# Kernel tuning notes

Measured on AMD Instinct MI355X. Metric: run time of the kernel, lower is better.

## Reference

```python
import jax, jax.numpy as jnp
import numpy as np

B, T, C = 2, 2048, 1024
H, DH = 16, 64            # n_head, head_size; H*DH == C
HID = 4096                # FFN hidden
EPS = 1e-5


def setup_inputs() -> dict:
    key = jax.random.key(0)
    ks = jax.random.split(key, 16)
    s_c = 1.0 / np.sqrt(C)
    s_h = 1.0 / np.sqrt(HID)
    return {
        "x": jax.random.normal(ks[0], (B, T, C), jnp.float32),
        "ln1_g": jnp.ones((C,), jnp.float32),
        "ln1_b": jnp.zeros((C,), jnp.float32),
        "Wq": jax.random.normal(ks[1], (H, C, DH), jnp.float32) * s_c,
        "Wk": jax.random.normal(ks[2], (H, C, DH), jnp.float32) * s_c,
        "Wv": jax.random.normal(ks[3], (H, C, DH), jnp.float32) * s_c,
        "Wo": jax.random.normal(ks[4], (C, C), jnp.float32) * s_c,
        "bo": jnp.zeros((C,), jnp.float32),
        "ln2_g": jnp.ones((C,), jnp.float32),
        "ln2_b": jnp.zeros((C,), jnp.float32),
        "W1": jax.random.normal(ks[5], (C, HID), jnp.float32) * s_c,
        "b1": jnp.zeros((HID,), jnp.float32),
        "W2": jax.random.normal(ks[6], (HID, C), jnp.float32) * s_h,
        "b2": jnp.zeros((C,), jnp.float32),
    }


def _layernorm(x, g, b):
    mu = jnp.mean(x, axis=-1, keepdims=True)
    var = jnp.mean(jnp.square(x - mu), axis=-1, keepdims=True)
    return (x - mu) * jax.lax.rsqrt(var + EPS) * g + b


def _block(x, ln1_g, ln1_b, Wq, Wk, Wv, Wo, bo, ln2_g, ln2_b, W1, b1, W2, b2):
    # --- self-attention (note: scale by C**-0.5, as in original code) ---
    h = _layernorm(x, ln1_g, ln1_b)                      # [B,T,C]
    q = jnp.einsum("btc,hcd->bhtd", h, Wq)
    k = jnp.einsum("btc,hcd->bhtd", h, Wk)
    v = jnp.einsum("btc,hcd->bhtd", h, Wv)
    wei = jnp.einsum("bhtd,bhsd->bhts", q, k) * (C ** -0.5)
    causal = jnp.tril(jnp.ones((T, T), bool))            # [T,T]
    wei = jnp.where(causal, wei, -jnp.inf)
    wei = jax.nn.softmax(wei, axis=-1)
    att = jnp.einsum("bhts,bhsd->bhtd", wei, v)          # [B,H,T,DH]
    att = att.transpose(0, 2, 1, 3).reshape(x.shape[0], x.shape[1], C)  # concat heads
    x = x + att @ Wo + bo
    # --- feed-forward ---
    h2 = _layernorm(x, ln2_g, ln2_b)
    x = x + jax.nn.relu(h2 @ W1 + b1) @ W2 + b2
    return x


def reference(x, ln1_g, ln1_b, Wq, Wk, Wv, Wo, bo, ln2_g, ln2_b, W1, b1, W2, b2):
    return _block(x, ln1_g, ln1_b, Wq, Wk, Wv, Wo, bo, ln2_g, ln2_b, W1, b1, W2, b2)
```

## Files before the change

kernel.cpp:

```cpp
#include <hip/hip_runtime.h>

typedef unsigned short ushort_t;
typedef __attribute__((ext_vector_type(8))) short short8;
typedef __attribute__((ext_vector_type(4))) float f32x4;

#define BT 4096
#define TSEQ 2048
#define CC 1024
#define NH 16
#define DH 64
#define HID 4096
#define ATT_SCALE 0.03125f

__device__ __forceinline__ ushort_t f2bf(float f) {
    unsigned u = __float_as_uint(f);
    u = u + 0x7fffu + ((u >> 16) & 1u);
    return (ushort_t)(u >> 16);
}
__device__ __forceinline__ float bf2f(ushort_t u) {
    return __uint_as_float(((unsigned)u) << 16);
}

typedef const __attribute__((address_space(1))) unsigned int* gptr_t;
typedef __attribute__((address_space(3))) unsigned int* lptr_t;
__device__ __forceinline__ void gload_lds16(const void* g, void* l) {
    __builtin_amdgcn_global_load_lds((gptr_t)g, (lptr_t)l, 16, 0, 0);
}

template <int N> __device__ __forceinline__ void vmcnt_wait() {
    if constexpr (N == 0)      asm volatile("s_waitcnt vmcnt(0)" ::: "memory");
    else if constexpr (N == 3) asm volatile("s_waitcnt vmcnt(3)" ::: "memory");
    else if constexpr (N == 4) asm volatile("s_waitcnt vmcnt(4)" ::: "memory");
    else if constexpr (N == 6) asm volatile("s_waitcnt vmcnt(6)" ::: "memory");
    else if constexpr (N == 8) asm volatile("s_waitcnt vmcnt(8)" ::: "memory");
    else static_assert(N == 0, "unsupported vmcnt");
}

__global__ __launch_bounds__(256) void transpose_cvt(
    const float* __restrict__ in, ushort_t* __restrict__ out, int R, int Cn)
{
    __shared__ float tile[32][33];
    size_t off = (size_t)blockIdx.z * R * Cn;
    int c0 = blockIdx.x * 32, r0 = blockIdx.y * 32;
    int tx = threadIdx.x & 31, ty = threadIdx.x >> 5;
#pragma unroll
    for (int q = 0; q < 4; ++q)
        tile[ty + 8 * q][tx] = in[off + (size_t)(r0 + ty + 8 * q) * Cn + c0 + tx];
    __syncthreads();
#pragma unroll
    for (int q = 0; q < 4; ++q)
        out[off + (size_t)(c0 + ty + 8 * q) * R + r0 + tx] = f2bf(tile[tx][ty + 8 * q]);
}

__global__ __launch_bounds__(256) void transpose_qkv(
    const float* __restrict__ Wq, const float* __restrict__ Wk,
    const float* __restrict__ Wv, ushort_t* __restrict__ WqkvT)
{
    __shared__ float tile[32][33];
    int z = blockIdx.z, mat = z >> 4, head = z & 15;
    const float* in = (mat == 0 ? Wq : (mat == 1 ? Wk : Wv)) + (size_t)head * CC * DH;
    ushort_t* out = WqkvT + (size_t)z * DH * CC;
    int c0 = blockIdx.x * 32, r0 = blockIdx.y * 32;
    int tx = threadIdx.x & 31, ty = threadIdx.x >> 5;
#pragma unroll
    for (int q = 0; q < 4; ++q)
        tile[ty + 8 * q][tx] = in[(size_t)(r0 + ty + 8 * q) * DH + c0 + tx];
    __syncthreads();
#pragma unroll
    for (int q = 0; q < 4; ++q)
        out[(size_t)(c0 + ty + 8 * q) * CC + r0 + tx] = f2bf(tile[tx][ty + 8 * q]);
}

__global__ __launch_bounds__(256) void ln_kernel(
    const float* __restrict__ x, const float* __restrict__ g,
    const float* __restrict__ b, ushort_t* __restrict__ out)
{
    int row = blockIdx.x;
    const float4 xv = ((const float4*)(x + (size_t)row * CC))[threadIdx.x];
    float s = xv.x + xv.y + xv.z + xv.w;
    float s2 = xv.x * xv.x + xv.y * xv.y + xv.z * xv.z + xv.w * xv.w;
#pragma unroll
    for (int d = 1; d < 64; d <<= 1) {
        s += __shfl_xor(s, d);
        s2 += __shfl_xor(s2, d);
    }
    __shared__ float ps[4], ps2[4];
    int w = threadIdx.x >> 6, lane = threadIdx.x & 63;
    if (lane == 0) { ps[w] = s; ps2[w] = s2; }
    __syncthreads();
    s = ps[0] + ps[1] + ps[2] + ps[3];
    s2 = ps2[0] + ps2[1] + ps2[2] + ps2[3];
    float mu = s * (1.0f / CC);
    float var = s2 * (1.0f / CC) - mu * mu;
    float rs = rsqrtf(var + 1e-5f);
    int c = threadIdx.x * 4;
    const float4 gv = ((const float4*)g)[threadIdx.x];
    const float4 bv = ((const float4*)b)[threadIdx.x];
    ushort_t u0 = f2bf((xv.x - mu) * rs * gv.x + bv.x);
    ushort_t u1 = f2bf((xv.y - mu) * rs * gv.y + bv.y);
    ushort_t u2 = f2bf((xv.z - mu) * rs * gv.z + bv.z);
    ushort_t u3 = f2bf((xv.w - mu) * rs * gv.w + bv.w);
    unsigned lo = (unsigned)u0 | ((unsigned)u1 << 16);
    unsigned hi = (unsigned)u2 | ((unsigned)u3 << 16);
    ((uint2*)(out + (size_t)row * CC + c))[0] = make_uint2(lo, hi);
}

template <int BM, int BN, int WM, int WN, int MR, int NR, int MODE, int D>
__global__ __launch_bounds__(256) void gemm_tile(
    const ushort_t* __restrict__ A, const ushort_t* __restrict__ Bt,
    int N, int K, int lda, int ldb,
    const float* __restrict__ bias, const float* __restrict__ resid,
    void* __restrict__ out0, void* __restrict__ out1, void* __restrict__ out2)
{
    static_assert(WM * WN == 4 && WM * MR * 16 == BM && WN * NR * 16 == BN, "geom");
    constexpr int L = BM / 64 + BN / 64;
    __shared__ ushort_t As[D][BM * 32];
    __shared__ ushort_t Bs[D][BN * 32];

    const int t = threadIdx.x;
    const int w = t >> 6, lane = t & 63, g = lane >> 4, c = lane & 15;
    const int wr = w / WN, wc = w % WN;
    const int m0 = blockIdx.x * BM;
    const int n0 = blockIdx.y * BN;
    if (MODE == 3) {
        A += (size_t)blockIdx.z * K;
        Bt += (size_t)blockIdx.z * K;
    }

    f32x4 acc[MR][NR];
#pragma unroll
    for (int mi = 0; mi < MR; ++mi)
#pragma unroll
        for (int ni = 0; ni < NR; ++ni) acc[mi][ni] = f32x4{0.f, 0.f, 0.f, 0.f};

    const int arow = t >> 2, acol = (t & 3) * 8;
    const int aoff = (wr * MR * 16 + c) * 32 + g * 8;
    const int boff = (wc * NR * 16 + c) * 32 + g * 8;

#define STAGE(BUF, K0)                                                          \
    {                                                                           \
        _Pragma("unroll") for (int j = 0; j < BM / 64; ++j)                     \
            gload_lds16(A + (size_t)(m0 + j * 64 + arow) * lda + (K0) + acol,   \
                        As[BUF] + (size_t)j * 2048 + t * 8);                    \
        _Pragma("unroll") for (int j = 0; j < BN / 64; ++j)                     \
            gload_lds16(Bt + (size_t)(n0 + j * 64 + arow) * ldb + (K0) + acol,  \
                        Bs[BUF] + (size_t)j * 2048 + t * 8);                    \
    }

    const int nt = K >> 5;
#pragma unroll
    for (int d = 0; d < D - 1; ++d) STAGE(d, d * 32);

    int cur = 0;
    for (int ti = 0; ti < nt; ++ti) {
        const int ahead = nt - 1 - ti;
        if (ahead >= D - 1) {
            const int stg = (cur == 0) ? D - 1 : cur - 1;
            STAGE(stg, (ti + D - 1) * 32);
            vmcnt_wait<(D - 1) * L>();
        } else if (D == 3 && ahead == 1) {
            vmcnt_wait<L>();
        } else {
            vmcnt_wait<0>();
        }
        __builtin_amdgcn_sched_barrier(0);
        __builtin_amdgcn_s_barrier();

        const ushort_t* Ard = As[cur] + aoff;
        const ushort_t* Brd = Bs[cur] + boff;
        short8 af[MR], bf[NR];
#pragma unroll
        for (int mi = 0; mi < MR; ++mi) af[mi] = *(const short8*)(Ard + mi * 512);
#pragma unroll
        for (int ni = 0; ni < NR; ++ni) bf[ni] = *(const short8*)(Brd + ni * 512);
        __builtin_amdgcn_s_setprio(1);
#pragma unroll
        for (int mi = 0; mi < MR; ++mi)
#pragma unroll
            for (int ni = 0; ni < NR; ++ni)
                acc[mi][ni] = __builtin_amdgcn_mfma_f32_16x16x32_bf16(
                    af[mi], bf[ni], acc[mi][ni], 0, 0, 0);
        __builtin_amdgcn_s_setprio(0);

        __builtin_amdgcn_sched_barrier(0);
        __builtin_amdgcn_s_barrier();
        cur = (cur + 1 == D) ? 0 : cur + 1;
    }
#undef STAGE

#pragma unroll
    for (int mi = 0; mi < MR; ++mi)
#pragma unroll
        for (int ni = 0; ni < NR; ++ni)
#pragma unroll
            for (int i = 0; i < 4; ++i) {
                int row = m0 + wr * MR * 16 + mi * 16 + g * 4 + i;
                int col = n0 + wc * NR * 16 + ni * 16 + c;
                float v = acc[mi][ni][i];
                if (MODE == 0) {
                    v += bias[col] + resid[(size_t)row * N + col];
                    ((float*)out0)[(size_t)row * N + col] = v;
                } else if (MODE == 1) {
                    v += bias[col];
                    v = v > 0.f ? v : 0.f;
                    ((ushort_t*)out0)[(size_t)row * N + col] = f2bf(v);
                } else if (MODE == 3) {
                    ((ushort_t*)out0)[(size_t)blockIdx.z * BT * N + (size_t)row * N + col] =
                        f2bf(v);
                } else {
                    int bb = row >> 11, tt = row & (TSEQ - 1);
                    if (col < 1024) {
                        int head = col >> 6, d = col & 63;
                        ((ushort_t*)out0)[((size_t)(bb * NH + head) * TSEQ + tt) * DH + d] =
                            f2bf(v * ATT_SCALE);
                    } else if (col < 2048) {
                        int head = (col - 1024) >> 6, d = col & 63;
                        ((ushort_t*)out1)[((size_t)(bb * NH + head) * TSEQ + tt) * DH + d] = f2bf(v);
                    } else {
                        int head = (col - 2048) >> 6, d = col & 63;
                        ((ushort_t*)out2)[((size_t)(bb * NH + head) * DH + d) * TSEQ + tt] = f2bf(v);
                    }
                }
            }
}

__global__ __launch_bounds__(256) void ffn2_combine(
    const ushort_t* __restrict__ parts, const float* __restrict__ bias,
    const float* __restrict__ resid, float* __restrict__ out)
{
    const size_t off = ((size_t)blockIdx.x * 256 + threadIdx.x) * 8;
    const int col = (int)(off & 1023);
    short8 p0 = *(const short8*)(parts + off);
    short8 p1 = *(const short8*)(parts + (size_t)BT * CC + off);
    float4 r0 = ((const float4*)(resid + off))[0];
    float4 r1 = ((const float4*)(resid + off + 4))[0];
    float4 b0 = ((const float4*)(bias + col))[0];
    float4 b1 = ((const float4*)(bias + col + 4))[0];
    float o[8];
#pragma unroll
    for (int j = 0; j < 8; ++j)
        o[j] = bf2f((ushort_t)p0[j]) + bf2f((ushort_t)p1[j]);
    float4 w0 = make_float4(o[0] + b0.x + r0.x, o[1] + b0.y + r0.y,
                            o[2] + b0.z + r0.z, o[3] + b0.w + r0.w);
    float4 w1 = make_float4(o[4] + b1.x + r1.x, o[5] + b1.y + r1.y,
                            o[6] + b1.z + r1.z, o[7] + b1.w + r1.w);
    ((float4*)(out + off))[0] = w0;
    ((float4*)(out + off + 4))[0] = w1;
}

__global__ __launch_bounds__(256) void flash_split(
    const ushort_t* __restrict__ Q, const ushort_t* __restrict__ Kb,
    const ushort_t* __restrict__ Vt, float* __restrict__ opart,
    float* __restrict__ mlpart, ushort_t* __restrict__ attout)
{
    __shared__ ushort_t Ks[64 * 64];
    __shared__ ushort_t Vs[64 * 64];
    __shared__ ushort_t Plds[4][16 * 72];
    const int t = threadIdx.x;
    const int w = t >> 6, lane = t & 63;
    const int g = lane >> 4, c = lane & 15;
    const int bh = blockIdx.x, qb = blockIdx.y, sc = blockIdx.z;
    if (sc * 8 > qb) return;
    const int bb = bh >> 4, hh = bh & 15;
    const int q0 = qb * 64 + w * 16;
    const ushort_t* qp = Q + (size_t)bh * TSEQ * DH;
    const char* kpB = (const char*)(Kb + (size_t)bh * TSEQ * DH);
    const char* vpB = (const char*)(Vt + (size_t)bh * DH * TSEQ);

    const short8 bq0 = *(const short8*)(qp + (size_t)(q0 + c) * DH + g * 8);
    const short8 bq1 = *(const short8*)(qp + (size_t)(q0 + c) * DH + 32 + g * 8);

    float m_ = -INFINITY, l_ = 0.f;
    f32x4 o[4];
#pragma unroll
    for (int nf = 0; nf < 4; ++nf) o[nf] = f32x4{0.f, 0.f, 0.f, 0.f};

    const int st0 = sc * 8;
    const int send = (st0 + 7 < qb) ? st0 + 7 : qb;
    ushort_t* pw = &Plds[w][c * 72];
    const unsigned bxor = (unsigned)((c & 7) << 4);

    const int srow = t >> 3, sb = (t & 7) * 16;
#define STAGE_KV(ST)                                                                \
    {                                                                               \
        const int S0_ = (ST) * 64;                                                  \
        _Pragma("unroll") for (int j = 0; j < 2; ++j) {                             \
            int r = j * 32 + srow;                                                  \
            int bs = sb ^ ((r & 7) << 4);                                           \
            gload_lds16(kpB + (size_t)(S0_ + r) * 128 + bs,                         \
                        (char*)Ks + r * 128 + sb);                                  \
            gload_lds16(vpB + (size_t)r * (TSEQ * 2) + S0_ * 2 + bs,                \
                        (char*)Vs + r * 128 + sb);                                  \
        }                                                                           \
    }

    STAGE_KV(st0);
    for (int st = st0; st <= send; ++st) {
        const int S0 = st * 64;
        __syncthreads();

        __builtin_amdgcn_s_setprio(1);
        f32x4 sa[4];
#pragma unroll
        for (int sub = 0; sub < 4; ++sub) {
            const char* kr = (const char*)Ks + (16 * sub + c) * 128;
            short8 k0 = *(const short8*)(kr + ((g * 16) ^ bxor));
            short8 k1 = *(const short8*)(kr + ((64 + g * 16) ^ bxor));
            f32x4 t0 = f32x4{0.f, 0.f, 0.f, 0.f};
            t0 = __builtin_amdgcn_mfma_f32_16x16x32_bf16(k0, bq0, t0, 0, 0, 0);
            t0 = __builtin_amdgcn_mfma_f32_16x16x32_bf16(k1, bq1, t0, 0, 0, 0);
            sa[sub] = t0;
        }
        __builtin_amdgcn_s_setprio(0);

        float pvv[16];
#pragma unroll
        for (int sub = 0; sub < 4; ++sub)
#pragma unroll
            for (int i = 0; i < 4; ++i) pvv[4 * sub + i] = sa[sub][i];
        if (st == qb) {
#pragma unroll
            for (int sub = 0; sub < 4; ++sub)
#pragma unroll
                for (int i = 0; i < 4; ++i)
                    if (S0 + 16 * sub + 4 * g + i > q0 + c) pvv[4 * sub + i] = -INFINITY;
        }
        float tmax = pvv[0];
#pragma unroll
        for (int j = 1; j < 16; ++j) tmax = fmaxf(tmax, pvv[j]);
        tmax = fmaxf(tmax, __shfl_xor(tmax, 16));
        tmax = fmaxf(tmax, __shfl_xor(tmax, 32));
        if (!__all(tmax - m_ <= 8.0f)) {
            float mn = fmaxf(m_, tmax);
            float fac = __expf(m_ - mn);
            m_ = mn;
            l_ *= fac;
#pragma unroll
            for (int i = 0; i < 4; ++i) {
                float fr = __shfl(fac, 4 * g + i);
#pragma unroll
                for (int nf = 0; nf < 4; ++nf) o[nf][i] *= fr;
            }
        }
        float pp[16], rs = 0.f;
#pragma unroll
        for (int j = 0; j < 16; ++j) { pp[j] = __expf(pvv[j] - m_); rs += pp[j]; }
        rs += __shfl_xor(rs, 16);
        rs += __shfl_xor(rs, 32);
        l_ += rs;

#pragma unroll
        for (int sub = 0; sub < 4; ++sub) {
            unsigned lo = (__float_as_uint(pp[4 * sub + 0]) >> 16) |
                          (__float_as_uint(pp[4 * sub + 1]) & 0xffff0000u);
            unsigned hi = (__float_as_uint(pp[4 * sub + 2]) >> 16) |
                          (__float_as_uint(pp[4 * sub + 3]) & 0xffff0000u);
            *(uint2*)(pw + 16 * sub + 4 * g) = make_uint2(lo, hi);
        }
        asm volatile("s_waitcnt lgkmcnt(0)" ::: "memory");
        short8 pa0 = *(const short8*)(&Plds[w][c * 72 + g * 8]);
        short8 pa1 = *(const short8*)(&Plds[w][c * 72 + 32 + g * 8]);

        __builtin_amdgcn_s_setprio(1);
#pragma unroll
        for (int nf = 0; nf < 4; ++nf) {
            const char* vr = (const char*)Vs + (nf * 16 + c) * 128;
            short8 v0 = *(const short8*)(vr + ((g * 16) ^ bxor));
            short8 v1 = *(const short8*)(vr + ((64 + g * 16) ^ bxor));
            o[nf] = __builtin_amdgcn_mfma_f32_16x16x32_bf16(pa0, v0, o[nf], 0, 0, 0);
            o[nf] = __builtin_amdgcn_mfma_f32_16x16x32_bf16(pa1, v1, o[nf], 0, 0, 0);
        }
        __builtin_amdgcn_s_setprio(0);

        __syncthreads();
        if (st < send) STAGE_KV(st + 1);
    }
#undef STAGE_KV

    if (qb < 8) {
#pragma unroll
        for (int i = 0; i < 4; ++i) {
            float rl = 1.0f / __shfl(l_, 4 * g + i);
            int tt = q0 + 4 * g + i;
#pragma unroll
            for (int nf = 0; nf < 4; ++nf)
                attout[((size_t)(bb * TSEQ + tt)) * CC + hh * DH + nf * 16 + c] =
                    f2bf(o[nf][i] * rl);
        }
    } else {
        const size_t slot = (size_t)(bh * 32 + qb) * 4 + sc;
        float* op = opart + slot * 4096;
#pragma unroll
        for (int nf = 0; nf < 4; ++nf)
#pragma unroll
            for (int i = 0; i < 4; ++i)
                op[(size_t)(w * 16 + 4 * g + i) * 64 + nf * 16 + c] = o[nf][i];
        if (g == 0) {
            mlpart[slot * 128 + w * 16 + c] = m_;
            mlpart[slot * 128 + 64 + w * 16 + c] = l_;
        }
    }
}

__global__ __launch_bounds__(256) void flash_combine(
    const float* __restrict__ opart, const float* __restrict__ mlpart,
    ushort_t* __restrict__ attout)
{
    const int bh = blockIdx.x, qb = blockIdx.y + 8;
    const int bb = bh >> 4, hh = bh & 15;
    const int nsc = (qb >> 3) + 1;
    const int t = threadIdx.x, r = t >> 2, qc = t & 3;
    const size_t slot0 = (size_t)(bh * 32 + qb) * 4;

    float mi[4], li[4];
    float M = -INFINITY;
#pragma unroll
    for (int i = 0; i < 4; ++i) {
        if (i < nsc) {
            mi[i] = mlpart[(slot0 + i) * 128 + r];
            li[i] = mlpart[(slot0 + i) * 128 + 64 + r];
            M = fmaxf(M, mi[i]);
        }
    }
    float L = 0.f;
    f32x4 acc[4];
#pragma unroll
    for (int j = 0; j < 4; ++j) acc[j] = f32x4{0.f, 0.f, 0.f, 0.f};
#pragma unroll
    for (int i = 0; i < 4; ++i) {
        if (i < nsc) {
            float F = __expf(mi[i] - M);
            L += li[i] * F;
            const f32x4* orow = (const f32x4*)(opart + (slot0 + i) * 4096 +
                                               (size_t)r * 64 + qc * 16);
#pragma unroll
            for (int j = 0; j < 4; ++j) acc[j] += orow[j] * F;
        }
    }
    float rl = 1.0f / L;
    unsigned wb[8];
#pragma unroll
    for (int j = 0; j < 4; ++j) {
        wb[2 * j] = (unsigned)f2bf(acc[j][0] * rl) | ((unsigned)f2bf(acc[j][1] * rl) << 16);
        wb[2 * j + 1] = (unsigned)f2bf(acc[j][2] * rl) | ((unsigned)f2bf(acc[j][3] * rl) << 16);
    }
    ushort_t* dst = attout + ((size_t)(bb * TSEQ + qb * 64 + r)) * CC + hh * DH + qc * 16;
    ((uint4*)dst)[0] = make_uint4(wb[0], wb[1], wb[2], wb[3]);
    ((uint4*)dst)[1] = make_uint4(wb[4], wb[5], wb[6], wb[7]);
}

extern "C" void kernel_launch(void* const* d_in, const int* in_sizes, int n_in,
                              void* d_out, int out_size, void* d_ws, size_t ws_size,
                              hipStream_t stream)
{
    (void)in_sizes; (void)n_in; (void)out_size; (void)ws_size;
    const float* x     = (const float*)d_in[0];
    const float* ln1_g = (const float*)d_in[1];
    const float* ln1_b = (const float*)d_in[2];
    const float* Wq    = (const float*)d_in[3];
    const float* Wk    = (const float*)d_in[4];
    const float* Wv    = (const float*)d_in[5];
    const float* Wo    = (const float*)d_in[6];
    const float* bo    = (const float*)d_in[7];
    const float* ln2_g = (const float*)d_in[8];
    const float* ln2_b = (const float*)d_in[9];
    const float* W1    = (const float*)d_in[10];
    const float* b1    = (const float*)d_in[11];
    const float* W2    = (const float*)d_in[12];
    const float* b2    = (const float*)d_in[13];

    char* p = (char*)d_ws;
    ushort_t* hbuf  = (ushort_t*)p;  p += (size_t)BT * CC * 2;
    ushort_t* WqkvT = (ushort_t*)p;  p += (size_t)3 * CC * CC * 2;
    ushort_t* WoT   = (ushort_t*)p;  p += (size_t)CC * CC * 2;
    ushort_t* W1T   = (ushort_t*)p;  p += (size_t)CC * HID * 2;
    ushort_t* W2T   = (ushort_t*)p;  p += (size_t)HID * CC * 2;
    ushort_t* Qb    = (ushort_t*)p;  p += (size_t)BT * CC * 2;
    ushort_t* Kbuf  = (ushort_t*)p;  p += (size_t)BT * CC * 2;
    ushort_t* Vt    = (ushort_t*)p;  p += (size_t)BT * CC * 2;
    ushort_t* atto  = (ushort_t*)p;  p += (size_t)BT * CC * 2;
    float*    x1    = (float*)p;     p += (size_t)BT * CC * 4;
    ushort_t* h2    = (ushort_t*)p;  p += (size_t)BT * CC * 2;
    ushort_t* mid   = (ushort_t*)p;  p += (size_t)BT * HID * 2;
    float*    opart = (float*)p;     p += (size_t)4096 * 4096 * 4;
    float*    mlprt = (float*)p;     p += (size_t)4096 * 128 * 4;

    dim3 blk(256);
    transpose_qkv<<<dim3(DH / 32, CC / 32, 3 * NH), blk, 0, stream>>>(Wq, Wk, Wv, WqkvT);
    transpose_cvt<<<dim3(CC / 32, CC / 32, 1), blk, 0, stream>>>(Wo, WoT, CC, CC);
    transpose_cvt<<<dim3(HID / 32, CC / 32, 1), blk, 0, stream>>>(W1, W1T, CC, HID);
    transpose_cvt<<<dim3(CC / 32, HID / 32, 1), blk, 0, stream>>>(W2, W2T, HID, CC);

    ln_kernel<<<dim3(BT), blk, 0, stream>>>(x, ln1_g, ln1_b, hbuf);
    gemm_tile<128, 128, 2, 2, 4, 4, 2, 2><<<dim3(BT / 128, 3072 / 128), blk, 0, stream>>>(
        hbuf, WqkvT, 3072, CC, CC, CC, nullptr, nullptr, Qb, Kbuf, Vt);
    flash_split<<<dim3(2 * NH, TSEQ / 64, 4), blk, 0, stream>>>(
        Qb, Kbuf, Vt, opart, mlprt, atto);
    flash_combine<<<dim3(2 * NH, TSEQ / 64 - 8), blk, 0, stream>>>(opart, mlprt, atto);
    gemm_tile<128, 64, 4, 1, 2, 4, 0, 3><<<dim3(BT / 128, CC / 64), blk, 0, stream>>>(
        atto, WoT, CC, CC, CC, CC, bo, x, (void*)x1, nullptr, nullptr);
    ln_kernel<<<dim3(BT), blk, 0, stream>>>(x1, ln2_g, ln2_b, h2);
    gemm_tile<128, 128, 2, 2, 4, 4, 1, 2><<<dim3(BT / 128, HID / 128), blk, 0, stream>>>(
        h2, W1T, HID, CC, CC, CC, b1, nullptr, (void*)mid, nullptr, nullptr);
    gemm_tile<128, 64, 4, 1, 2, 4, 3, 3><<<dim3(BT / 128, CC / 64, 2), blk, 0, stream>>>(
        mid, W2T, CC, HID / 2, HID, HID, nullptr, nullptr, (void*)opart, nullptr, nullptr);
    ffn2_combine<<<dim3(BT * CC / 8 / 256), blk, 0, stream>>>(
        (const ushort_t*)opart, b2, x1, (float*)d_out);
}
```

Measured before the change: 253.5 us.

## Add 256x256 XOR-swizzled 512-thread GEMM for QKV, FFN1 and split-K FFN2

Adds a new GEMM kernel with 256x256 output tiles, 512 threads (8 waves), BK=64 double buffering, and an XOR-swizzled LDS layout that avoids bank conflicts. It is used for the QKV projection, FFN up-projection and FFN down-projection. The down-projection split-K goes from 2 to 4 splits so the grid stays large enough, and the combine kernel now sums four bf16 partials. The bigger tiles raise data reuse per block, at the cost of more registers and LDS per block, fewer blocks for the smaller GEMMs, and an extra partial-sum read and bf16 rounding in the combine step.

```diff
diff --git a/kernel.cpp b/kernel.cpp
--- a/kernel.cpp
+++ b/kernel.cpp
@@ -105,102 +105,114 @@
     ((uint2*)(out + (size_t)row * CC + c))[0] = make_uint2(lo, hi);
 }
 
-template <int BM, int BN, int WM, int WN, int MR, int NR, int MODE, int D>
-__global__ __launch_bounds__(256) void gemm_tile(
+template <int MODE>
+__global__ __launch_bounds__(512) void gemm256(
     const ushort_t* __restrict__ A, const ushort_t* __restrict__ Bt,
-    int N, int K, int lda, int ldb,
-    const float* __restrict__ bias, const float* __restrict__ resid,
+    int N, int K, int lda, int ldb, const float* __restrict__ bias,
     void* __restrict__ out0, void* __restrict__ out1, void* __restrict__ out2)
 {
-    static_assert(WM * WN == 4 && WM * MR * 16 == BM && WN * NR * 16 == BN, "geom");
-    constexpr int L = BM / 64 + BN / 64;
-    __shared__ ushort_t As[D][BM * 32];
-    __shared__ ushort_t Bs[D][BN * 32];
+    __shared__ ushort_t As[2][256 * 64];
+    __shared__ ushort_t Bs[2][256 * 64];
 
     const int t = threadIdx.x;
-    const int w = t >> 6, lane = t & 63, g = lane >> 4, c = lane & 15;
-    const int wr = w / WN, wc = w % WN;
-    const int m0 = blockIdx.x * BM;
-    const int n0 = blockIdx.y * BN;
+    const int wid = t >> 6, lane = t & 63, g = lane >> 4, c = lane & 15;
+    const int wr = wid >> 2, wc = wid & 3;
+    const int m0 = blockIdx.x * 256;
+    const int n0 = blockIdx.y * 256;
     if (MODE == 3) {
         A += (size_t)blockIdx.z * K;
         Bt += (size_t)blockIdx.z * K;
     }
 
-    f32x4 acc[MR][NR];
-#pragma unroll
-    for (int mi = 0; mi < MR; ++mi)
-#pragma unroll
-        for (int ni = 0; ni < NR; ++ni) acc[mi][ni] = f32x4{0.f, 0.f, 0.f, 0.f};
-
-    const int arow = t >> 2, acol = (t & 3) * 8;
-    const int aoff = (wr * MR * 16 + c) * 32 + g * 8;
-    const int boff = (wc * NR * 16 + c) * 32 + g * 8;
-
-#define STAGE(BUF, K0)                                                          \
-    {                                                                           \
-        _Pragma("unroll") for (int j = 0; j < BM / 64; ++j)                     \
-            gload_lds16(A + (size_t)(m0 + j * 64 + arow) * lda + (K0) + acol,   \
-                        As[BUF] + (size_t)j * 2048 + t * 8);                    \
-        _Pragma("unroll") for (int j = 0; j < BN / 64; ++j)                     \
-            gload_lds16(Bt + (size_t)(n0 + j * 64 + arow) * ldb + (K0) + acol,  \
-                        Bs[BUF] + (size_t)j * 2048 + t * 8);                    \
-    }
-
-    const int nt = K >> 5;
-#pragma unroll
-    for (int d = 0; d < D - 1; ++d) STAGE(d, d * 32);
-
-    int cur = 0;
+    f32x4 acc[8][4];
+#pragma unroll
+    for (int am = 0; am < 8; ++am)
+#pragma unroll
+        for (int an = 0; an < 4; ++an) acc[am][an] = f32x4{0.f, 0.f, 0.f, 0.f};
+
+    const int srow = t >> 3, sbyte = (t & 7) * 16;
+    const unsigned rxor = (unsigned)((c & 7) << 4);
+
+#define STAGE256(BUF, TI)                                                          \
+    {                                                                              \
+        _Pragma("unroll") for (int j = 0; j < 4; ++j) {                            \
+            int r = j * 64 + srow;                                                 \
+            int bs = sbyte ^ ((r & 7) << 4);                                       \
+            gload_lds16((const char*)A + ((size_t)(m0 + r) * lda + (size_t)(TI) * 64) * 2 + bs, \
+                        (char*)As[BUF] + r * 128 + sbyte);                         \
+            gload_lds16((const char*)Bt + ((size_t)(n0 + r) * ldb + (size_t)(TI) * 64) * 2 + bs, \
+                        (char*)Bs[BUF] + r * 128 + sbyte);                         \
+        }                                                                          \
+    }
+
+    const int nt = K >> 6;
+    STAGE256(0, 0);
     for (int ti = 0; ti < nt; ++ti) {
-        const int ahead = nt - 1 - ti;
-        if (ahead >= D - 1) {
-            const int stg = (cur == 0) ? D - 1 : cur - 1;
-            STAGE(stg, (ti + D - 1) * 32);
-            vmcnt_wait<(D - 1) * L>();
-        } else if (D == 3 && ahead == 1) {
-            vmcnt_wait<L>();
+        const int cur = ti & 1;
+        if (ti + 1 < nt) {
+            STAGE256(cur ^ 1, ti + 1);
+            vmcnt_wait<8>();
         } else {
             vmcnt_wait<0>();
         }
         __builtin_amdgcn_sched_barrier(0);
         __builtin_amdgcn_s_barrier();
-
-        const ushort_t* Ard = As[cur] + aoff;
-        const ushort_t* Brd = Bs[cur] + boff;
-        short8 af[MR], bf[NR];
-#pragma unroll
-        for (int mi = 0; mi < MR; ++mi) af[mi] = *(const short8*)(Ard + mi * 512);
-#pragma unroll
-        for (int ni = 0; ni < NR; ++ni) bf[ni] = *(const short8*)(Brd + ni * 512);
-        __builtin_amdgcn_s_setprio(1);
-#pragma unroll
-        for (int mi = 0; mi < MR; ++mi)
-#pragma unroll
-            for (int ni = 0; ni < NR; ++ni)
-                acc[mi][ni] = __builtin_amdgcn_mfma_f32_16x16x32_bf16(
-                    af[mi], bf[ni], acc[mi][ni], 0, 0, 0);
-        __builtin_amdgcn_s_setprio(0);
-
+        __builtin_amdgcn_sched_barrier(0);
+
+        short8 af[4][2], bf[2][2];
+#pragma unroll
+        for (int mh = 0; mh < 2; ++mh) {
+#pragma unroll
+            for (int mi = 0; mi < 4; ++mi) {
+                int ra = wr * 128 + mh * 64 + mi * 16 + c;
+#pragma unroll
+                for (int ks = 0; ks < 2; ++ks)
+                    af[mi][ks] = *(const short8*)((const char*)As[cur] + ra * 128 +
+                                                  (((unsigned)(ks * 64 + g * 16)) ^ rxor));
+            }
+#pragma unroll
+            for (int nh = 0; nh < 2; ++nh) {
+#pragma unroll
+                for (int ni = 0; ni < 2; ++ni) {
+                    int rb = wc * 64 + nh * 32 + ni * 16 + c;
+#pragma unroll
+                    for (int ks = 0; ks < 2; ++ks)
+                        bf[ni][ks] = *(const short8*)((const char*)Bs[cur] + rb * 128 +
+                                                      (((unsigned)(ks * 64 + g * 16)) ^ rxor));
+                }
+                __builtin_amdgcn_s_setprio(1);
+#pragma unroll
+                for (int mi = 0; mi < 4; ++mi)
+#pragma unroll
+                    for (int ni = 0; ni < 2; ++ni)
+#pragma unroll
+                        for (int ks = 0; ks < 2; ++ks)
+                            acc[mh * 4 + mi][nh * 2 + ni] =
+                                __builtin_amdgcn_mfma_f32_16x16x32_bf16(
+                                    af[mi][ks], bf[ni][ks], acc[mh * 4 + mi][nh * 2 + ni],
+                                    0, 0, 0);
+                __builtin_amdgcn_s_setprio(0);
+                if (!(mh == 1 && nh == 1)) {
+                    __builtin_amdgcn_sched_barrier(0);
+                    __builtin_amdgcn_s_barrier();
+                }
+            }
+        }
         __builtin_amdgcn_sched_barrier(0);
         __builtin_amdgcn_s_barrier();
-        cur = (cur + 1 == D) ? 0 : cur + 1;
-    }
-#undef STAGE
-
-#pragma unroll
-    for (int mi = 0; mi < MR; ++mi)
-#pragma unroll
-        for (int ni = 0; ni < NR; ++ni)
+    }
+#undef STAGE256
+
+#pragma unroll
+    for (int am = 0; am < 8; ++am)
+#pragma unroll
+        for (int an = 0; an < 4; ++an)
 #pragma unroll
             for (int i = 0; i < 4; ++i) {
-                int row = m0 + wr * MR * 16 + mi * 16 + g * 4 + i;
-                int col = n0 + wc * NR * 16 + ni * 16 + c;
-                float v = acc[mi][ni][i];
-                if (MODE == 0) {
-                    v += bias[col] + resid[(size_t)row * N + col];
-                    ((float*)out0)[(size_t)row * N + col] = v;
-                } else if (MODE == 1) {
+                int row = m0 + wr * 128 + am * 16 + g * 4 + i;
+                int col = n0 + wc * 64 + an * 16 + c;
+                float v = acc[am][an][i];
+                if (MODE == 1) {
                     v += bias[col];
                     v = v > 0.f ? v : 0.f;
                     ((ushort_t*)out0)[(size_t)row * N + col] = f2bf(v);
@@ -224,6 +236,98 @@
             }
 }
 
+template <int BM, int BN, int WM, int WN, int MR, int NR, int MODE, int D>
+__global__ __launch_bounds__(256) void gemm_tile(
+    const ushort_t* __restrict__ A, const ushort_t* __restrict__ Bt,
+    int N, int K, int lda, int ldb,
+    const float* __restrict__ bias, const float* __restrict__ resid,
+    void* __restrict__ out0)
+{
+    static_assert(WM * WN == 4 && WM * MR * 16 == BM && WN * NR * 16 == BN, "geom");
+    constexpr int L = BM / 64 + BN / 64;
+    __shared__ ushort_t As[D][BM * 32];
+    __shared__ ushort_t Bs[D][BN * 32];
+
+    const int t = threadIdx.x;
+    const int w = t >> 6, lane = t & 63, g = lane >> 4, c = lane & 15;
+    const int wr = w / WN, wc = w % WN;
+    const int m0 = blockIdx.x * BM;
+    const int n0 = blockIdx.y * BN;
+
+    f32x4 acc[MR][NR];
+#pragma unroll
+    for (int mi = 0; mi < MR; ++mi)
+#pragma unroll
+        for (int ni = 0; ni < NR; ++ni) acc[mi][ni] = f32x4{0.f, 0.f, 0.f, 0.f};
+
+    const int arow = t >> 2, acol = (t & 3) * 8;
+    const int aoff = (wr * MR * 16 + c) * 32 + g * 8;
+    const int boff = (wc * NR * 16 + c) * 32 + g * 8;
+
+#define STAGE(BUF, K0)                                                          \
+    {                                                                           \
+        _Pragma("unroll") for (int j = 0; j < BM / 64; ++j)                     \
+            gload_lds16(A + (size_t)(m0 + j * 64 + arow) * lda + (K0) + acol,   \
+                        As[BUF] + (size_t)j * 2048 + t * 8);                    \
+        _Pragma("unroll") for (int j = 0; j < BN / 64; ++j)                     \
+            gload_lds16(Bt + (size_t)(n0 + j * 64 + arow) * ldb + (K0) + acol,  \
+                        Bs[BUF] + (size_t)j * 2048 + t * 8);                    \
+    }
+
+    const int nt = K >> 5;
+#pragma unroll
+    for (int d = 0; d < D - 1; ++d) STAGE(d, d * 32);
+
+    int cur = 0;
+    for (int ti = 0; ti < nt; ++ti) {
+        const int ahead = nt - 1 - ti;
+        if (ahead >= D - 1) {
+            const int stg = (cur == 0) ? D - 1 : cur - 1;
+            STAGE(stg, (ti + D - 1) * 32);
+            vmcnt_wait<(D - 1) * L>();
+        } else if (D == 3 && ahead == 1) {
+            vmcnt_wait<L>();
+        } else {
+            vmcnt_wait<0>();
+        }
+        __builtin_amdgcn_sched_barrier(0);
+        __builtin_amdgcn_s_barrier();
+
+        const ushort_t* Ard = As[cur] + aoff;
+        const ushort_t* Brd = Bs[cur] + boff;
+        short8 af[MR], bf[NR];
+#pragma unroll
+        for (int mi = 0; mi < MR; ++mi) af[mi] = *(const short8*)(Ard + mi * 512);
+#pragma unroll
+        for (int ni = 0; ni < NR; ++ni) bf[ni] = *(const short8*)(Brd + ni * 512);
+        __builtin_amdgcn_s_setprio(1);
+#pragma unroll
+        for (int mi = 0; mi < MR; ++mi)
+#pragma unroll
+            for (int ni = 0; ni < NR; ++ni)
+                acc[mi][ni] = __builtin_amdgcn_mfma_f32_16x16x32_bf16(
+                    af[mi], bf[ni], acc[mi][ni], 0, 0, 0);
+        __builtin_amdgcn_s_setprio(0);
+
+        __builtin_amdgcn_sched_barrier(0);
+        __builtin_amdgcn_s_barrier();
+        cur = (cur + 1 == D) ? 0 : cur + 1;
+    }
+#undef STAGE
+
+#pragma unroll
+    for (int mi = 0; mi < MR; ++mi)
+#pragma unroll
+        for (int ni = 0; ni < NR; ++ni)
+#pragma unroll
+            for (int i = 0; i < 4; ++i) {
+                int row = m0 + wr * MR * 16 + mi * 16 + g * 4 + i;
+                int col = n0 + wc * NR * 16 + ni * 16 + c;
+                float v = acc[mi][ni][i] + bias[col] + resid[(size_t)row * N + col];
+                ((float*)out0)[(size_t)row * N + col] = v;
+            }
+}
+
 __global__ __launch_bounds__(256) void ffn2_combine(
     const ushort_t* __restrict__ parts, const float* __restrict__ bias,
     const float* __restrict__ resid, float* __restrict__ out)
@@ -232,6 +336,8 @@
     const int col = (int)(off & 1023);
     short8 p0 = *(const short8*)(parts + off);
     short8 p1 = *(const short8*)(parts + (size_t)BT * CC + off);
+    short8 p2 = *(const short8*)(parts + (size_t)2 * BT * CC + off);
+    short8 p3 = *(const short8*)(parts + (size_t)3 * BT * CC + off);
     float4 r0 = ((const float4*)(resid + off))[0];
     float4 r1 = ((const float4*)(resid + off + 4))[0];
     float4 b0 = ((const float4*)(bias + col))[0];
@@ -239,7 +345,8 @@
     float o[8];
 #pragma unroll
     for (int j = 0; j < 8; ++j)
-        o[j] = bf2f((ushort_t)p0[j]) + bf2f((ushort_t)p1[j]);
+        o[j] = bf2f((ushort_t)p0[j]) + bf2f((ushort_t)p1[j]) +
+               bf2f((ushort_t)p2[j]) + bf2f((ushort_t)p3[j]);
     float4 w0 = make_float4(o[0] + b0.x + r0.x, o[1] + b0.y + r0.y,
                             o[2] + b0.z + r0.z, o[3] + b0.w + r0.w);
     float4 w1 = make_float4(o[4] + b1.x + r1.x, o[5] + b1.y + r1.y,
@@ -492,18 +599,18 @@
     transpose_cvt<<<dim3(CC / 32, HID / 32, 1), blk, 0, stream>>>(W2, W2T, HID, CC);
 
     ln_kernel<<<dim3(BT), blk, 0, stream>>>(x, ln1_g, ln1_b, hbuf);
-    gemm_tile<128, 128, 2, 2, 4, 4, 2, 2><<<dim3(BT / 128, 3072 / 128), blk, 0, stream>>>(
-        hbuf, WqkvT, 3072, CC, CC, CC, nullptr, nullptr, Qb, Kbuf, Vt);
+    gemm256<2><<<dim3(BT / 256, 3072 / 256), dim3(512), 0, stream>>>(
+        hbuf, WqkvT, 3072, CC, CC, CC, nullptr, Qb, Kbuf, Vt);
     flash_split<<<dim3(2 * NH, TSEQ / 64, 4), blk, 0, stream>>>(
         Qb, Kbuf, Vt, opart, mlprt, atto);
     flash_combine<<<dim3(2 * NH, TSEQ / 64 - 8), blk, 0, stream>>>(opart, mlprt, atto);
     gemm_tile<128, 64, 4, 1, 2, 4, 0, 3><<<dim3(BT / 128, CC / 64), blk, 0, stream>>>(
-        atto, WoT, CC, CC, CC, CC, bo, x, (void*)x1, nullptr, nullptr);
+        atto, WoT, CC, CC, CC, CC, bo, x, (void*)x1);
     ln_kernel<<<dim3(BT), blk, 0, stream>>>(x1, ln2_g, ln2_b, h2);
-    gemm_tile<128, 128, 2, 2, 4, 4, 1, 2><<<dim3(BT / 128, HID / 128), blk, 0, stream>>>(
-        h2, W1T, HID, CC, CC, CC, b1, nullptr, (void*)mid, nullptr, nullptr);
-    gemm_tile<128, 64, 4, 1, 2, 4, 3, 3><<<dim3(BT / 128, CC / 64, 2), blk, 0, stream>>>(
-        mid, W2T, CC, HID / 2, HID, HID, nullptr, nullptr, (void*)opart, nullptr, nullptr);
+    gemm256<1><<<dim3(BT / 256, HID / 256), dim3(512), 0, stream>>>(
+        h2, W1T, HID, CC, CC, CC, b1, (void*)mid, nullptr, nullptr);
+    gemm256<3><<<dim3(BT / 256, CC / 256, 4), dim3(512), 0, stream>>>(
+        mid, W2T, CC, HID / 4, HID, HID, nullptr, (void*)opart, nullptr, nullptr);
     ffn2_combine<<<dim3(BT * CC / 8 / 256), blk, 0, stream>>>(
         (const ushort_t*)opart, b2, x1, (float*)d_out);
 }
```

Result: slower. 264.0 us (+4.2%).

## Add 256x256 eight-wave swizzled GEMM for QKV, FFN1 and split-K FFN2

Applied to the files above, without the earlier changes.

Adds a 512-thread GEMM with 256x256 output tiles and a K-step of 64. It uses an XOR-swizzled LDS layout and double buffering, and interleaves its global-to-LDS loads across four MFMA quarter-phases. This kernel replaces the 128x128 tiles in the QKV, FFN1 and FFN2 GEMMs, which should raise arithmetic intensity and cut redundant global loads. FFN2 moves from split-K 2 to split-K 4 to keep enough blocks in flight with the larger tiles, so the combine kernel now sums four bf16 partials. The cost is more barriers per iteration, heavy register use (128 accumulator registers per lane), and extra partial traffic and bf16 rounding from the wider split.

```diff
diff --git a/kernel.cpp b/kernel.cpp
--- a/kernel.cpp
+++ b/kernel.cpp
@@ -29,12 +29,17 @@
 
 template <int N> __device__ __forceinline__ void vmcnt_wait() {
     if constexpr (N == 0)      asm volatile("s_waitcnt vmcnt(0)" ::: "memory");
+    else if constexpr (N == 2) asm volatile("s_waitcnt vmcnt(2)" ::: "memory");
     else if constexpr (N == 3) asm volatile("s_waitcnt vmcnt(3)" ::: "memory");
     else if constexpr (N == 4) asm volatile("s_waitcnt vmcnt(4)" ::: "memory");
     else if constexpr (N == 6) asm volatile("s_waitcnt vmcnt(6)" ::: "memory");
-    else if constexpr (N == 8) asm volatile("s_waitcnt vmcnt(8)" ::: "memory");
     else static_assert(N == 0, "unsupported vmcnt");
 }
+
+#define LGKM0 do { asm volatile("s_waitcnt lgkmcnt(0)" ::: "memory"); \
+                   __builtin_amdgcn_sched_barrier(0); } while (0)
+#define SBAR  do { __builtin_amdgcn_sched_barrier(0); \
+                   __builtin_amdgcn_s_barrier(); } while (0)
 
 __global__ __launch_bounds__(256) void transpose_cvt(
     const float* __restrict__ in, ushort_t* __restrict__ out, int R, int Cn)
@@ -105,102 +110,118 @@
     ((uint2*)(out + (size_t)row * CC + c))[0] = make_uint2(lo, hi);
 }
 
-template <int BM, int BN, int WM, int WN, int MR, int NR, int MODE, int D>
-__global__ __launch_bounds__(256) void gemm_tile(
+template <int MODE>
+__global__ __launch_bounds__(512) void gemm256(
     const ushort_t* __restrict__ A, const ushort_t* __restrict__ Bt,
-    int N, int K, int lda, int ldb,
-    const float* __restrict__ bias, const float* __restrict__ resid,
+    int N, int K, int lda, int ldb, const float* __restrict__ bias,
     void* __restrict__ out0, void* __restrict__ out1, void* __restrict__ out2)
 {
-    static_assert(WM * WN == 4 && WM * MR * 16 == BM && WN * NR * 16 == BN, "geom");
-    constexpr int L = BM / 64 + BN / 64;
-    __shared__ ushort_t As[D][BM * 32];
-    __shared__ ushort_t Bs[D][BN * 32];
+    __shared__ char AsB[2][32768];
+    __shared__ char BsB[2][32768];
 
     const int t = threadIdx.x;
-    const int w = t >> 6, lane = t & 63, g = lane >> 4, c = lane & 15;
-    const int wr = w / WN, wc = w % WN;
-    const int m0 = blockIdx.x * BM;
-    const int n0 = blockIdx.y * BN;
+    const int wid = t >> 6, lane = t & 63, g = lane >> 4, c = lane & 15;
+    const int wr = wid >> 2, wc = wid & 3;
+    const int m0 = blockIdx.x * 256;
+    const int n0 = blockIdx.y * 256;
     if (MODE == 3) {
         A += (size_t)blockIdx.z * K;
         Bt += (size_t)blockIdx.z * K;
     }
 
-    f32x4 acc[MR][NR];
-#pragma unroll
-    for (int mi = 0; mi < MR; ++mi)
-#pragma unroll
-        for (int ni = 0; ni < NR; ++ni) acc[mi][ni] = f32x4{0.f, 0.f, 0.f, 0.f};
-
-    const int arow = t >> 2, acol = (t & 3) * 8;
-    const int aoff = (wr * MR * 16 + c) * 32 + g * 8;
-    const int boff = (wc * NR * 16 + c) * 32 + g * 8;
-
-#define STAGE(BUF, K0)                                                          \
-    {                                                                           \
-        _Pragma("unroll") for (int j = 0; j < BM / 64; ++j)                     \
-            gload_lds16(A + (size_t)(m0 + j * 64 + arow) * lda + (K0) + acol,   \
-                        As[BUF] + (size_t)j * 2048 + t * 8);                    \
-        _Pragma("unroll") for (int j = 0; j < BN / 64; ++j)                     \
-            gload_lds16(Bt + (size_t)(n0 + j * 64 + arow) * ldb + (K0) + acol,  \
-                        Bs[BUF] + (size_t)j * 2048 + t * 8);                    \
-    }
-
-    const int nt = K >> 5;
-#pragma unroll
-    for (int d = 0; d < D - 1; ++d) STAGE(d, d * 32);
-
-    int cur = 0;
+    f32x4 acc[8][4];
+#pragma unroll
+    for (int am = 0; am < 8; ++am)
+#pragma unroll
+        for (int an = 0; an < 4; ++an) acc[am][an] = f32x4{0.f, 0.f, 0.f, 0.f};
+
+    const int srow = t >> 3, sbyte = (t & 7) * 16;
+    const int rbB = (wc & 1) * 64;
+    short8 af[4][2], bf[2][2];
+
+#define STG(PTR, LD, BROW, DST, HOFF, TI)                                        \
+    { _Pragma("unroll") for (int j = 0; j < 2; ++j) {                            \
+        int r = j * 64 + srow;                                                   \
+        int bs = sbyte ^ ((r & 7) << 4);                                         \
+        gload_lds16((const char*)(PTR) +                                         \
+                        ((size_t)((BROW) + r) * (LD) + (size_t)(TI) * 64) * 2 + bs, \
+                    (DST) + (HOFF) + r * 128 + sbyte); } }
+
+#define DSAF(BUF, MH)                                                            \
+    { const char* ab = AsB[BUF] + wr * 16384;                                    \
+      _Pragma("unroll") for (int mi = 0; mi < 4; ++mi) {                         \
+        int ra = (MH) * 64 + mi * 16 + c;                                        \
+        _Pragma("unroll") for (int ks = 0; ks < 2; ++ks)                         \
+            af[mi][ks] = *(const short8*)(ab + ra * 128 +                        \
+                (((unsigned)(ks * 64 + g * 16)) ^ ((unsigned)((ra & 7) << 4)))); } }
+
+#define DSBF(BUF, NH)                                                            \
+    { const char* bb = BsB[BUF] + (wc >> 1) * 16384;                             \
+      _Pragma("unroll") for (int ni = 0; ni < 2; ++ni) {                         \
+        int rb = rbB + (NH) * 32 + ni * 16 + c;                                  \
+        _Pragma("unroll") for (int ks = 0; ks < 2; ++ks)                         \
+            bf[ni][ks] = *(const short8*)(bb + rb * 128 +                        \
+                (((unsigned)(ks * 64 + g * 16)) ^ ((unsigned)((rb & 7) << 4)))); } }
+
+#define MFMAQ(MH, NH)                                                            \
+    __builtin_amdgcn_s_setprio(1);                                               \
+    _Pragma("unroll") for (int mi = 0; mi < 4; ++mi)                             \
+    _Pragma("unroll") for (int ni = 0; ni < 2; ++ni)                             \
+    _Pragma("unroll") for (int ks = 0; ks < 2; ++ks)                             \
+        acc[(MH) * 4 + mi][(NH) * 2 + ni] = __builtin_amdgcn_mfma_f32_16x16x32_bf16( \
+            af[mi][ks], bf[ni][ks], acc[(MH) * 4 + mi][(NH) * 2 + ni], 0, 0, 0); \
+    __builtin_amdgcn_s_setprio(0);
+
+    const int nt = K >> 6;
+    STG(A,  lda, m0,        AsB[0], 0,     0);
+    STG(A,  lda, m0 + 128,  AsB[0], 16384, 0);
+    STG(Bt, ldb, n0,        BsB[0], 0,     0);
+    STG(Bt, ldb, n0 + 128,  BsB[0], 16384, 0);
+
     for (int ti = 0; ti < nt; ++ti) {
-        const int ahead = nt - 1 - ti;
-        if (ahead >= D - 1) {
-            const int stg = (cur == 0) ? D - 1 : cur - 1;
-            STAGE(stg, (ti + D - 1) * 32);
-            vmcnt_wait<(D - 1) * L>();
-        } else if (D == 3 && ahead == 1) {
-            vmcnt_wait<L>();
-        } else {
-            vmcnt_wait<0>();
-        }
-        __builtin_amdgcn_sched_barrier(0);
-        __builtin_amdgcn_s_barrier();
-
-        const ushort_t* Ard = As[cur] + aoff;
-        const ushort_t* Brd = Bs[cur] + boff;
-        short8 af[MR], bf[NR];
-#pragma unroll
-        for (int mi = 0; mi < MR; ++mi) af[mi] = *(const short8*)(Ard + mi * 512);
-#pragma unroll
-        for (int ni = 0; ni < NR; ++ni) bf[ni] = *(const short8*)(Brd + ni * 512);
-        __builtin_amdgcn_s_setprio(1);
-#pragma unroll
-        for (int mi = 0; mi < MR; ++mi)
-#pragma unroll
-            for (int ni = 0; ni < NR; ++ni)
-                acc[mi][ni] = __builtin_amdgcn_mfma_f32_16x16x32_bf16(
-                    af[mi], bf[ni], acc[mi][ni], 0, 0, 0);
-        __builtin_amdgcn_s_setprio(0);
-
-        __builtin_amdgcn_sched_barrier(0);
-        __builtin_amdgcn_s_barrier();
-        cur = (cur + 1 == D) ? 0 : cur + 1;
-    }
-#undef STAGE
-
-#pragma unroll
-    for (int mi = 0; mi < MR; ++mi)
-#pragma unroll
-        for (int ni = 0; ni < NR; ++ni)
+        const int b = ti & 1, nb = b ^ 1;
+        const bool more = (ti + 1 < nt);
+        if (more) { STG(A, lda, m0, AsB[nb], 0, ti + 1); vmcnt_wait<2>(); }
+        else        vmcnt_wait<0>();
+        SBAR;
+        DSAF(b, 0); DSBF(b, 0);
+        LGKM0;
+        MFMAQ(0, 0);
+        SBAR;
+        if (more) STG(A, lda, m0 + 128, AsB[nb], 16384, ti + 1);
+        DSBF(b, 1);
+        SBAR;
+        LGKM0;
+        MFMAQ(0, 1);
+        SBAR;
+        if (more) STG(Bt, ldb, n0, BsB[nb], 0, ti + 1);
+        DSAF(b, 1); DSBF(b, 0);
+        SBAR;
+        LGKM0;
+        MFMAQ(1, 0);
+        SBAR;
+        if (more) STG(Bt, ldb, n0 + 128, BsB[nb], 16384, ti + 1);
+        DSBF(b, 1);
+        SBAR;
+        LGKM0;
+        MFMAQ(1, 1);
+        SBAR;
+    }
+#undef STG
+#undef DSAF
+#undef DSBF
+#undef MFMAQ
+
+#pragma unroll
+    for (int am = 0; am < 8; ++am)
+#pragma unroll
+        for (int an = 0; an < 4; ++an)
 #pragma unroll
             for (int i = 0; i < 4; ++i) {
-                int row = m0 + wr * MR * 16 + mi * 16 + g * 4 + i;
-                int col = n0 + wc * NR * 16 + ni * 16 + c;
-                float v = acc[mi][ni][i];
-                if (MODE == 0) {
-                    v += bias[col] + resid[(size_t)row * N + col];
-                    ((float*)out0)[(size_t)row * N + col] = v;
-                } else if (MODE == 1) {
+                int row = m0 + wr * 128 + am * 16 + g * 4 + i;
+                int col = n0 + wc * 64 + an * 16 + c;
+                float v = acc[am][an][i];
+                if (MODE == 1) {
                     v += bias[col];
                     v = v > 0.f ? v : 0.f;
                     ((ushort_t*)out0)[(size_t)row * N + col] = f2bf(v);
@@ -224,6 +245,96 @@
             }
 }
 
+template <int BM, int BN, int WM, int WN, int MR, int NR, int MODE, int D>
+__global__ __launch_bounds__(256) void gemm_tile(
+    const ushort_t* __restrict__ A, const ushort_t* __restrict__ Bt,
+    int N, int K, int lda, int ldb,
+    const float* __restrict__ bias, const float* __restrict__ resid,
+    void* __restrict__ out0)
+{
+    static_assert(WM * WN == 4 && WM * MR * 16 == BM && WN * NR * 16 == BN, "geom");
+    constexpr int L = BM / 64 + BN / 64;
+    __shared__ ushort_t As[D][BM * 32];
+    __shared__ ushort_t Bs[D][BN * 32];
+
+    const int t = threadIdx.x;
+    const int w = t >> 6, lane = t & 63, g = lane >> 4, c = lane & 15;
+    const int wr = w / WN, wc = w % WN;
+    const int m0 = blockIdx.x * BM;
+    const int n0 = blockIdx.y * BN;
+
+    f32x4 acc[MR][NR];
+#pragma unroll
+    for (int mi = 0; mi < MR; ++mi)
+#pragma unroll
+        for (int ni = 0; ni < NR; ++ni) acc[mi][ni] = f32x4{0.f, 0.f, 0.f, 0.f};
+
+    const int arow = t >> 2, acol = (t & 3) * 8;
+    const int aoff = (wr * MR * 16 + c) * 32 + g * 8;
+    const int boff = (wc * NR * 16 + c) * 32 + g * 8;
+
+#define STAGE(BUF, K0)                                                          \
+    {                                                                           \
+        _Pragma("unroll") for (int j = 0; j < BM / 64; ++j)                     \
+            gload_lds16(A + (size_t)(m0 + j * 64 + arow) * lda + (K0) + acol,   \
+                        As[BUF] + (size_t)j * 2048 + t * 8);                    \
+        _Pragma("unroll") for (int j = 0; j < BN / 64; ++j)                     \
+            gload_lds16(Bt + (size_t)(n0 + j * 64 + arow) * ldb + (K0) + acol,  \
+                        Bs[BUF] + (size_t)j * 2048 + t * 8);                    \
+    }
+
+    const int nt = K >> 5;
+#pragma unroll
+    for (int d = 0; d < D - 1; ++d) STAGE(d, d * 32);
+
+    int cur = 0;
+    for (int ti = 0; ti < nt; ++ti) {
+        const int ahead = nt - 1 - ti;
+        if (ahead >= D - 1) {
+            const int stg = (cur == 0) ? D - 1 : cur - 1;
+            STAGE(stg, (ti + D - 1) * 32);
+            vmcnt_wait<(D - 1) * L>();
+        } else if (D == 3 && ahead == 1) {
+            vmcnt_wait<L>();
+        } else {
+            vmcnt_wait<0>();
+        }
+        SBAR;
+
+        const ushort_t* Ard = As[cur] + aoff;
+        const ushort_t* Brd = Bs[cur] + boff;
+        short8 af[MR], bf[NR];
+#pragma unroll
+        for (int mi = 0; mi < MR; ++mi) af[mi] = *(const short8*)(Ard + mi * 512);
+#pragma unroll
+        for (int ni = 0; ni < NR; ++ni) bf[ni] = *(const short8*)(Brd + ni * 512);
+        __builtin_amdgcn_s_setprio(1);
+#pragma unroll
+        for (int mi = 0; mi < MR; ++mi)
+#pragma unroll
+            for (int ni = 0; ni < NR; ++ni)
+                acc[mi][ni] = __builtin_amdgcn_mfma_f32_16x16x32_bf16(
+                    af[mi], bf[ni], acc[mi][ni], 0, 0, 0);
+        __builtin_amdgcn_s_setprio(0);
+
+        SBAR;
+        cur = (cur + 1 == D) ? 0 : cur + 1;
+    }
+#undef STAGE
+
+#pragma unroll
+    for (int mi = 0; mi < MR; ++mi)
+#pragma unroll
+        for (int ni = 0; ni < NR; ++ni)
+#pragma unroll
+            for (int i = 0; i < 4; ++i) {
+                int row = m0 + wr * MR * 16 + mi * 16 + g * 4 + i;
+                int col = n0 + wc * NR * 16 + ni * 16 + c;
+                float v = acc[mi][ni][i] + bias[col] + resid[(size_t)row * N + col];
+                ((float*)out0)[(size_t)row * N + col] = v;
+            }
+}
+
 __global__ __launch_bounds__(256) void ffn2_combine(
     const ushort_t* __restrict__ parts, const float* __restrict__ bias,
     const float* __restrict__ resid, float* __restrict__ out)
@@ -232,6 +343,8 @@
     const int col = (int)(off & 1023);
     short8 p0 = *(const short8*)(parts + off);
     short8 p1 = *(const short8*)(parts + (size_t)BT * CC + off);
+    short8 p2 = *(const short8*)(parts + (size_t)2 * BT * CC + off);
+    short8 p3 = *(const short8*)(parts + (size_t)3 * BT * CC + off);
     float4 r0 = ((const float4*)(resid + off))[0];
     float4 r1 = ((const float4*)(resid + off + 4))[0];
     float4 b0 = ((const float4*)(bias + col))[0];
@@ -239,7 +352,8 @@
     float o[8];
 #pragma unroll
     for (int j = 0; j < 8; ++j)
-        o[j] = bf2f((ushort_t)p0[j]) + bf2f((ushort_t)p1[j]);
+        o[j] = bf2f((ushort_t)p0[j]) + bf2f((ushort_t)p1[j]) +
+               bf2f((ushort_t)p2[j]) + bf2f((ushort_t)p3[j]);
     float4 w0 = make_float4(o[0] + b0.x + r0.x, o[1] + b0.y + r0.y,
                             o[2] + b0.z + r0.z, o[3] + b0.w + r0.w);
     float4 w1 = make_float4(o[4] + b1.x + r1.x, o[5] + b1.y + r1.y,
@@ -492,18 +606,18 @@
     transpose_cvt<<<dim3(CC / 32, HID / 32, 1), blk, 0, stream>>>(W2, W2T, HID, CC);
 
     ln_kernel<<<dim3(BT), blk, 0, stream>>>(x, ln1_g, ln1_b, hbuf);
-    gemm_tile<128, 128, 2, 2, 4, 4, 2, 2><<<dim3(BT / 128, 3072 / 128), blk, 0, stream>>>(
-        hbuf, WqkvT, 3072, CC, CC, CC, nullptr, nullptr, Qb, Kbuf, Vt);
+    gemm256<2><<<dim3(BT / 256, 3072 / 256), dim3(512), 0, stream>>>(
+        hbuf, WqkvT, 3072, CC, CC, CC, nullptr, Qb, Kbuf, Vt);
     flash_split<<<dim3(2 * NH, TSEQ / 64, 4), blk, 0, stream>>>(
         Qb, Kbuf, Vt, opart, mlprt, atto);
     flash_combine<<<dim3(2 * NH, TSEQ / 64 - 8), blk, 0, stream>>>(opart, mlprt, atto);
     gemm_tile<128, 64, 4, 1, 2, 4, 0, 3><<<dim3(BT / 128, CC / 64), blk, 0, stream>>>(
-        atto, WoT, CC, CC, CC, CC, bo, x, (void*)x1, nullptr, nullptr);
+        atto, WoT, CC, CC, CC, CC, bo, x, (void*)x1);
     ln_kernel<<<dim3(BT), blk, 0, stream>>>(x1, ln2_g, ln2_b, h2);
-    gemm_tile<128, 128, 2, 2, 4, 4, 1, 2><<<dim3(BT / 128, HID / 128), blk, 0, stream>>>(
-        h2, W1T, HID, CC, CC, CC, b1, nullptr, (void*)mid, nullptr, nullptr);
-    gemm_tile<128, 64, 4, 1, 2, 4, 3, 3><<<dim3(BT / 128, CC / 64, 2), blk, 0, stream>>>(
-        mid, W2T, CC, HID / 2, HID, HID, nullptr, nullptr, (void*)opart, nullptr, nullptr);
+    gemm256<1><<<dim3(BT / 256, HID / 256), dim3(512), 0, stream>>>(
+        h2, W1T, HID, CC, CC, CC, b1, (void*)mid, nullptr, nullptr);
+    gemm256<3><<<dim3(BT / 256, CC / 256, 4), dim3(512), 0, stream>>>(
+        mid, W2T, CC, HID / 4, HID, HID, nullptr, (void*)opart, nullptr, nullptr);
     ffn2_combine<<<dim3(BT * CC / 8 / 256), blk, 0, stream>>>(
         (const ushort_t*)opart, b2, x1, (float*)d_out);
 }
```

Result: slower. 289.5 us (+14.2%).
